# Performance work log

Measured on AMD Instinct MI355X. Metric: run time of the kernel, lower is better.

The kernel has to match this reference:

```python
import jax, jax.numpy as jnp
import numpy as np

DIM = 128
HIDDEN = 512
T_END = 1.0
N_STEPS = 32  # fixed-step RK4 in place of adaptive dopri5


def setup_inputs() -> dict:
    key = jax.random.key(0)
    ks = jax.random.split(key, 8)
    d, h = DIM, HIDDEN
    x = jax.random.normal(ks[0], (65536, d), dtype=jnp.float32)
    # Rademacher probe vector for the Hutchinson trace estimator (fixed per forward pass)
    v = jnp.sign(jax.random.normal(ks[1], (65536, d), dtype=jnp.float32))
    v = jnp.where(v == 0, 1.0, v)
    # ODEF: MLP on concat([z, t]) -> hidden -> hidden -> dim, tanh activations
    s1 = 1.0 / np.sqrt(d + 1)
    s2 = 1.0 / np.sqrt(h)
    W1 = jax.random.uniform(ks[2], (d + 1, h), jnp.float32, -s1, s1)
    b1 = jnp.zeros((h,), jnp.float32)
    W2 = jax.random.uniform(ks[3], (h, h), jnp.float32, -s2, s2)
    b2 = jnp.zeros((h,), jnp.float32)
    W3 = jax.random.uniform(ks[4], (h, d), jnp.float32, -s2, s2)
    b3 = jnp.zeros((d,), jnp.float32)
    return {"x": x, "v": v, "W1": W1, "b1": b1, "W2": W2, "b2": b2, "W3": W3, "b3": b3}


def _mlp(t, z, W1, b1, W2, b2, W3, b3):
    # z: [B, D], t: scalar -> f(z, t): [B, D]
    tt = jnp.full((z.shape[0], 1), t, dtype=z.dtype)
    h = jnp.tanh(jnp.concatenate([z, tt], axis=1) @ W1 + b1)
    h = jnp.tanh(h @ W2 + b2)
    return h @ W3 + b3


def _dynamics(t, z, v, params):
    # returns dz/dt = f and dlogp/dt = -Tr(df/dz) ~= -(v^T J) . v
    f, vjp_fn = jax.vjp(lambda zz: _mlp(t, zz, *params), z)
    (vJ,) = vjp_fn(v)
    div = jnp.sum(vJ * v, axis=1)  # [B]
    return f, -div


def _integrate(x, v, params):
    dt = T_END / N_STEPS
    logp0 = jnp.zeros((x.shape[0],), x.dtype)

    def rk4_step(carry, i):
        z, lp = carry
        t = i.astype(x.dtype) * dt
        k1f, k1d = _dynamics(t, z, v, params)
        k2f, k2d = _dynamics(t + 0.5 * dt, z + 0.5 * dt * k1f, v, params)
        k3f, k3d = _dynamics(t + 0.5 * dt, z + 0.5 * dt * k2f, v, params)
        k4f, k4d = _dynamics(t + dt, z + dt * k3f, v, params)
        z_new = z + (dt / 6.0) * (k1f + 2.0 * k2f + 2.0 * k3f + k4f)
        lp_new = lp + (dt / 6.0) * (k1d + 2.0 * k2d + 2.0 * k3d + k4d)
        return (z_new, lp_new), None

    (zT, logpT), _ = jax.lax.scan(rk4_step, (x, logp0), jnp.arange(N_STEPS))
    return zT, logpT


def reference(x, v, W1, b1, W2, b2, W3, b3):
    params = (W1, b1, W2, b2, W3, b3)
    zT, logpT = _integrate(x, v, params)
    d = x.shape[1]
    log2pi = jnp.asarray(np.log(2.0 * np.pi), x.dtype)
    prior_lp = -0.5 * jnp.sum(zT * zT, axis=1) - 0.5 * d * log2pi  # N(0, I) log-density
    return prior_lp + logpT  # [B] log p(x)
```

## Files before the change

kernel.cpp:

```cpp
#include <hip/hip_runtime.h>


#define DIMV 128
#define HIDV 512
#define HS_STRIDE 520

typedef float  floatx4 __attribute__((ext_vector_type(4)));
typedef short  short8  __attribute__((ext_vector_type(8)));

static __device__ __forceinline__ unsigned short f2bf(float x) {
    union { float f; unsigned int u; } c; c.f = x;
    unsigned int u = c.u;
    u += 0x7FFFu + ((u >> 16) & 1u);
    return (unsigned short)(u >> 16);
}
static __device__ __forceinline__ float bf2f(unsigned short h) {
    union { unsigned int u; float f; } c; c.u = ((unsigned int)h) << 16;
    return c.f;
}
static __device__ __forceinline__ float fast_tanh(float x) {
    x = fminf(8.0f, fmaxf(-8.0f, x));
    float e = exp2f(x * 2.8853900817779268f);
    return (e - 1.0f) * __builtin_amdgcn_rcpf(e + 1.0f);
}

__global__ void pack_kernel(const float* __restrict__ src, unsigned short* __restrict__ dst,
                            int K, int N, int ld, int transpose) {
    int i = blockIdx.x * 256 + threadIdx.x;
    if (i >= K * N) return;
    int j  = i & 7;
    int n  = (i >> 3) % N;
    int k8 = (i >> 3) / N;
    int k  = k8 * 8 + j;
    float v = transpose ? src[n * ld + k] : src[k * ld + n];
    dst[i] = f2bf(v);
}

__global__ void init_k(const float* __restrict__ x, float* __restrict__ z,
                       unsigned short* __restrict__ zs, float* __restrict__ lp,
                       int n, int nrows) {
    int i = blockIdx.x * 256 + threadIdx.x;
    if (i < n) { float val = x[i]; z[i] = val; zs[i] = f2bf(val); }
    if (i < nrows) lp[i] = 0.0f;
}

#define PROD_BF16 0
#define PROD_V    1
#define EPI_H1   0
#define EPI_G3   1

struct GArgs {
    const float* v;
    const unsigned short* A;
    const unsigned short* Wp;
    const float* bias;
    const float* w1t;
    unsigned short* out0;
    float t;
};

template<int KDIM, int NDIM, int NFRAG, int PROD, int EPI>
__global__ __launch_bounds__(256, 2) void gemm_k(GArgs p) {
    __shared__ __align__(16) unsigned short As[128 * 72];
    const int tid  = threadIdx.x;
    const int wave = tid >> 6, lane = tid & 63;
    const int quad = lane >> 4, l16 = lane & 15;
    const int row0 = blockIdx.x * 128;
    const int colw = blockIdx.y * (NFRAG * 64) + wave * (NFRAG * 16);

    floatx4 acc[8][NFRAG];
    #pragma unroll
    for (int m = 0; m < 8; ++m)
        #pragma unroll
        for (int f = 0; f < NFRAG; ++f) {
            floatx4 zz = {0.f, 0.f, 0.f, 0.f};
            acc[m][f] = zz;
        }

    for (int k0 = 0; k0 < KDIM; k0 += 64) {
        __syncthreads();
        {
            const int r  = tid >> 3;
            const int cc = (tid & 7) << 3;
            #pragma unroll
            for (int i = 0; i < 4; ++i) {
                const int rr = r + (i << 5);
                const size_t base = (size_t)(row0 + rr) * KDIM + k0 + cc;
                if constexpr (PROD == PROD_BF16) {
                    const short8 val = *reinterpret_cast<const short8*>(&p.A[base]);
                    *reinterpret_cast<short8*>(&As[rr * 72 + cc]) = val;
                } else {
                    float vals[8];
                    *(float4*)&vals[0] = *(const float4*)&p.v[base];
                    *(float4*)&vals[4] = *(const float4*)&p.v[base + 4];
                    short8 sv;
                    #pragma unroll
                    for (int j = 0; j < 8; ++j) sv[j] = (short)f2bf(vals[j]);
                    *reinterpret_cast<short8*>(&As[rr * 72 + cc]) = sv;
                }
            }
        }
        __syncthreads();
        #pragma unroll
        for (int kt = 0; kt < 2; ++kt) {
            const int k8 = (k0 >> 3) + (kt << 2) + quad;
            short8 b[NFRAG];
            #pragma unroll
            for (int f = 0; f < NFRAG; ++f)
                b[f] = *reinterpret_cast<const short8*>(
                    &p.Wp[((size_t)k8 * NDIM + colw + (f << 4) + l16) << 3]);
            #pragma unroll
            for (int m = 0; m < 8; ++m) {
                const short8 a = *reinterpret_cast<const short8*>(
                    &As[(m * 16 + l16) * 72 + (kt << 5) + (quad << 3)]);
                #pragma unroll
                for (int f = 0; f < NFRAG; ++f)
                    acc[m][f] = __builtin_amdgcn_mfma_f32_16x16x32_bf16(a, b[f], acc[m][f], 0, 0, 0);
            }
        }
    }

    #pragma unroll
    for (int m = 0; m < 8; ++m)
        #pragma unroll
        for (int f = 0; f < NFRAG; ++f) {
            const int col = colw + (f << 4) + l16;
            float bias = 0.0f;
            if constexpr (EPI == EPI_H1) bias = p.bias[col] + p.t * p.w1t[col];
            #pragma unroll
            for (int r = 0; r < 4; ++r) {
                const int row = row0 + m * 16 + quad * 4 + r;
                const size_t idxN = (size_t)row * NDIM + col;
                float x = acc[m][f][r] + bias;
                if constexpr (EPI == EPI_H1) p.out0[idxN] = f2bf(fast_tanh(x));
                else                         p.out0[idxN] = f2bf(x);
            }
        }
}

struct FArgs {
    const unsigned short* A;
    const unsigned short* W2p;
    const unsigned short* W3p;
    const unsigned short* W2Tp;
    const unsigned short* g3;
    const unsigned short* u;
    const float* b2;
    const float* b3;
    float* z;
    float* accf;
    unsigned short* zs;
    float* accd;
    float* lp;
    float cnext, wrk;
    int s0, s3;
};

__global__ __launch_bounds__(512, 4) void kbc_k(FArgs p) {
    __shared__ __align__(16) unsigned short As[64 * 72];
    __shared__ __align__(16) unsigned short Hs[64 * HS_STRIDE];
    const int tid  = threadIdx.x;
    const int wave = tid >> 6, lane = tid & 63;
    const int quad = lane >> 4, l16 = lane & 15;
    const int row0 = blockIdx.x * 64;
    const int colw = wave << 6;

    floatx4 acc[4][4];
    #pragma unroll
    for (int m = 0; m < 4; ++m)
        #pragma unroll
        for (int f = 0; f < 4; ++f) { floatx4 zz = {0.f,0.f,0.f,0.f}; acc[m][f] = zz; }

    const int sr = tid >> 3;
    const int sc = (tid & 7) << 3;
    const unsigned short* Abase = p.A + (size_t)(row0 + sr) * 512 + sc;
    short8 st = *reinterpret_cast<const short8*>(Abase);

    for (int k0 = 0; k0 < 512; k0 += 64) {
        __syncthreads();
        *reinterpret_cast<short8*>(&As[sr * 72 + sc]) = st;
        if (k0 + 64 < 512)
            st = *reinterpret_cast<const short8*>(Abase + k0 + 64);
        __syncthreads();
        #pragma unroll
        for (int kt = 0; kt < 2; ++kt) {
            const int k8 = (k0 >> 3) + (kt << 2) + quad;
            short8 b[4];
            #pragma unroll
            for (int f = 0; f < 4; ++f)
                b[f] = *reinterpret_cast<const short8*>(
                    &p.W2p[((size_t)k8 * 512 + colw + (f << 4) + l16) << 3]);
            #pragma unroll
            for (int m = 0; m < 4; ++m) {
                const short8 a = *reinterpret_cast<const short8*>(
                    &As[(m * 16 + l16) * 72 + (kt << 5) + (quad << 3)]);
                #pragma unroll
                for (int f = 0; f < 4; ++f)
                    acc[m][f] = __builtin_amdgcn_mfma_f32_16x16x32_bf16(a, b[f], acc[m][f], 0, 0, 0);
            }
        }
    }
    #pragma unroll
    for (int m = 0; m < 4; ++m)
        #pragma unroll
        for (int f = 0; f < 4; ++f) {
            const int col = colw + (f << 4) + l16;
            const float bias = p.b2[col];
            #pragma unroll
            for (int r = 0; r < 4; ++r) {
                const int row = m * 16 + quad * 4 + r;
                Hs[row * HS_STRIDE + col] = f2bf(fast_tanh(acc[m][f][r] + bias));
            }
        }
    __syncthreads();

    {
        const int mB   = (wave & 3) << 4;
        const int half = (wave >> 2) << 6;
        floatx4 a3[4];
        #pragma unroll
        for (int f = 0; f < 4; ++f) { floatx4 zz = {0.f,0.f,0.f,0.f}; a3[f] = zz; }
        #pragma unroll 4
        for (int kt = 0; kt < 16; ++kt) {
            const int k8 = (kt << 2) + quad;
            short8 b[4];
            #pragma unroll
            for (int f = 0; f < 4; ++f)
                b[f] = *reinterpret_cast<const short8*>(
                    &p.W3p[((size_t)k8 * 128 + half + (f << 4) + l16) << 3]);
            const short8 a = *reinterpret_cast<const short8*>(
                &Hs[(mB + l16) * HS_STRIDE + (kt << 5) + (quad << 3)]);
            #pragma unroll
            for (int f = 0; f < 4; ++f)
                a3[f] = __builtin_amdgcn_mfma_f32_16x16x32_bf16(a, b[f], a3[f], 0, 0, 0);
        }
        #pragma unroll
        for (int f = 0; f < 4; ++f) {
            const int col = half + (f << 4) + l16;
            const float bias = p.b3[col];
            #pragma unroll
            for (int r = 0; r < 4; ++r) {
                const int row = row0 + mB + quad * 4 + r;
                const size_t idxN = (size_t)row * 128 + col;
                const float x = a3[f][r] + bias;
                const float a = p.wrk * x + (p.s0 ? 0.0f : p.accf[idxN]);
                if (p.s3) {
                    const float zn = p.z[idxN] + a;
                    p.z[idxN]  = zn;
                    p.zs[idxN] = f2bf(zn);
                } else {
                    p.accf[idxN] = a;
                    p.zs[idxN]   = f2bf(p.z[idxN] + p.cnext * x);
                }
            }
        }
    }
    __syncthreads();

    {
        const size_t gbase = (size_t)(row0 + sr) * 512;
        #pragma unroll
        for (int j = 0; j < 8; ++j) {
            const int cc = sc + (j << 6);
            short8 hv = *reinterpret_cast<const short8*>(&Hs[sr * HS_STRIDE + cc]);
            const short8 gv = *reinterpret_cast<const short8*>(&p.g3[gbase + cc]);
            short8 ov;
            #pragma unroll
            for (int e = 0; e < 8; ++e) {
                const float h = bf2f((unsigned short)hv[e]);
                const float g = bf2f((unsigned short)gv[e]);
                ov[e] = (short)f2bf(g * (1.0f - h * h));
            }
            *reinterpret_cast<short8*>(&Hs[sr * HS_STRIDE + cc]) = ov;
        }
    }
    __syncthreads();

    #pragma unroll
    for (int m = 0; m < 4; ++m)
        #pragma unroll
        for (int f = 0; f < 4; ++f) { floatx4 zz = {0.f,0.f,0.f,0.f}; acc[m][f] = zz; }
    #pragma unroll 2
    for (int kt = 0; kt < 16; ++kt) {
        const int k8 = (kt << 2) + quad;
        short8 b[4];
        #pragma unroll
        for (int f = 0; f < 4; ++f)
            b[f] = *reinterpret_cast<const short8*>(
                &p.W2Tp[((size_t)k8 * 512 + colw + (f << 4) + l16) << 3]);
        #pragma unroll
        for (int m = 0; m < 4; ++m) {
            const short8 a = *reinterpret_cast<const short8*>(
                &Hs[(m * 16 + l16) * HS_STRIDE + (kt << 5) + (quad << 3)]);
            #pragma unroll
            for (int f = 0; f < 4; ++f)
                acc[m][f] = __builtin_amdgcn_mfma_f32_16x16x32_bf16(a, b[f], acc[m][f], 0, 0, 0);
        }
    }
    __syncthreads();
    #pragma unroll
    for (int m = 0; m < 4; ++m)
        #pragma unroll
        for (int f = 0; f < 4; ++f) {
            const int col = colw + (f << 4) + l16;
            #pragma unroll
            for (int r = 0; r < 4; ++r) {
                const int row = m * 16 + quad * 4 + r;
                Hs[row * HS_STRIDE + col] = f2bf(acc[m][f][r]);
            }
        }
    __syncthreads();

    {
        const size_t gbase = (size_t)(row0 + sr) * 512;
        float s = 0.0f;
        #pragma unroll
        for (int j = 0; j < 8; ++j) {
            const int cc = sc + (j << 6);
            const short8 xv = *reinterpret_cast<const short8*>(&Hs[sr * HS_STRIDE + cc]);
            const short8 hv = *reinterpret_cast<const short8*>(&p.A[gbase + cc]);
            const short8 uv = *reinterpret_cast<const short8*>(&p.u[gbase + cc]);
            #pragma unroll
            for (int e = 0; e < 8; ++e) {
                const float x = bf2f((unsigned short)xv[e]);
                const float h = bf2f((unsigned short)hv[e]);
                const float uu = bf2f((unsigned short)uv[e]);
                s += x * (1.0f - h * h) * uu;
            }
        }
        s += __shfl_xor(s, 1);
        s += __shfl_xor(s, 2);
        s += __shfl_xor(s, 4);
        if ((tid & 7) == 0) {
            const int row = row0 + sr;
            const float a = p.wrk * (-s) + (p.s0 ? 0.0f : p.accd[row]);
            if (p.s3) p.lp[row] += a;
            else      p.accd[row] = a;
        }
    }
}

__global__ void final_k(const float* __restrict__ z, const float* __restrict__ lp,
                        float* __restrict__ out) {
    const int tid = threadIdx.x;
    const int row = blockIdx.x * 16 + (tid >> 4);
    const int l16 = tid & 15;
    const float4* zr = (const float4*)&z[(size_t)row * 128 + (l16 << 3)];
    float4 a = zr[0], b = zr[1];
    float s = a.x*a.x + a.y*a.y + a.z*a.z + a.w*a.w
            + b.x*b.x + b.y*b.y + b.z*b.z + b.w*b.w;
    s += __shfl_xor(s, 1);
    s += __shfl_xor(s, 2);
    s += __shfl_xor(s, 4);
    s += __shfl_xor(s, 8);
    if (l16 == 0) out[row] = lp[row] - 0.5f * s - 117.6241322501981f;
}

extern "C" void kernel_launch(void* const* d_in, const int* in_sizes, int n_in,
                              void* d_out, int out_size, void* d_ws, size_t ws_size,
                              hipStream_t stream) {
    (void)n_in; (void)out_size;
    const float* x  = (const float*)d_in[0];
    const float* v  = (const float*)d_in[1];
    const float* W1 = (const float*)d_in[2];
    const float* b1 = (const float*)d_in[3];
    const float* W2 = (const float*)d_in[4];
    const float* b2 = (const float*)d_in[5];
    const float* W3 = (const float*)d_in[6];
    const float* b3 = (const float*)d_in[7];
    float* out = (float*)d_out;
    const int B = in_sizes[0] / DIMV;

    auto al = [](size_t s) { return (s + 255) & ~(size_t)255; };
    auto need_for = [&](size_t C) {
        size_t s = 0;
        s += al(C * DIMV * 4);
        s += al(C * DIMV * 4);
        s += al(C * DIMV * 2);
        s += al(C * 4);
        s += al(C * 4);
        s += al(C * HIDV * 2) * 3;
        s += al(128 * 512 * 2) * 3 + al(512 * 512 * 2) * 2;
        return s;
    };
    size_t C = 32768;
    while (C > 1024 && need_for(C) > ws_size) C >>= 1;
    if (need_for(C) > ws_size) return;

    char* w = (char*)d_ws;
    auto alloc = [&](size_t bytes) { char* p = w; w += al(bytes); return p; };
    float* z    = (float*)alloc(C * DIMV * 4);
    float* accf = (float*)alloc(C * DIMV * 4);
    unsigned short* zs = (unsigned short*)alloc(C * DIMV * 2);
    float* lp   = (float*)alloc(C * 4);
    float* accd = (float*)alloc(C * 4);
    unsigned short* h1 = (unsigned short*)alloc(C * HIDV * 2);
    unsigned short* g3 = (unsigned short*)alloc(C * HIDV * 2);
    unsigned short* u  = (unsigned short*)alloc(C * HIDV * 2);
    unsigned short* W1zp  = (unsigned short*)alloc(128 * 512 * 2);
    unsigned short* W3p   = (unsigned short*)alloc(512 * 128 * 2);
    unsigned short* W3Tp  = (unsigned short*)alloc(128 * 512 * 2);
    unsigned short* W2p   = (unsigned short*)alloc(512 * 512 * 2);
    unsigned short* W2Tp  = (unsigned short*)alloc(512 * 512 * 2);

    auto pack = [&](const float* src, unsigned short* dst, int K, int N, int ld, int tr) {
        pack_kernel<<<dim3((K * N + 255) / 256), dim3(256), 0, stream>>>(src, dst, K, N, ld, tr);
    };
    pack(W1, W1zp,  128, 512, 512, 0);
    pack(W2, W2p,   512, 512, 512, 0);
    pack(W3, W3p,   512, 128, 128, 0);
    pack(W2, W2Tp,  512, 512, 512, 1);
    pack(W3, W3Tp,  128, 512, 128, 1);

    const float dt = 1.0f / 32.0f;
    const float cs[4]  = {0.0f, 0.5f * dt, 0.5f * dt, dt};
    const float wr4[4] = {dt / 6.0f, dt / 3.0f, dt / 3.0f, dt / 6.0f};
    const int GM128 = (int)C / 128;
    const int GMF   = (int)C / 64;

    for (int c0 = 0; c0 < B; c0 += (int)C) {
        const float* xc = x + (size_t)c0 * DIMV;
        const float* vc = v + (size_t)c0 * DIMV;

        init_k<<<dim3(((int)C * DIMV + 255) / 256), 256, 0, stream>>>(
            xc, z, zs, lp, (int)C * DIMV, (int)C);

        {
            GArgs p{};
            p.v = vc; p.Wp = W3Tp; p.out0 = g3;
            gemm_k<128, 512, 4, PROD_V, EPI_G3><<<dim3(GM128, 2), 256, 0, stream>>>(p);
            p.Wp = W1zp; p.out0 = u;
            gemm_k<128, 512, 4, PROD_V, EPI_G3><<<dim3(GM128, 2), 256, 0, stream>>>(p);
        }

        for (int step = 0; step < 32; ++step) {
            const float t0 = (float)step * dt;
            for (int s = 0; s < 4; ++s) {
                GArgs p{};
                p.t = t0 + cs[s];
                p.A = zs; p.Wp = W1zp; p.bias = b1; p.w1t = W1 + 128 * 512; p.out0 = h1;
                gemm_k<128, 512, 4, PROD_BF16, EPI_H1><<<dim3(GM128, 2), 256, 0, stream>>>(p);

                FArgs q{};
                q.A = h1; q.W2p = W2p; q.W3p = W3p; q.W2Tp = W2Tp;
                q.g3 = g3; q.u = u; q.b2 = b2; q.b3 = b3;
                q.z = z; q.accf = accf; q.zs = zs; q.accd = accd; q.lp = lp;
                q.cnext = (s < 3) ? cs[s + 1] : 0.0f;
                q.wrk = wr4[s];
                q.s0 = (s == 0); q.s3 = (s == 3);
                kbc_k<<<dim3(GMF), 512, 0, stream>>>(q);
            }
        }

        final_k<<<dim3((int)C / 16), 256, 0, stream>>>(z, lp, out + c0);
    }
}
```

Before: 22.03 ms.

## Fuse all RK4 stages into one persistent ODE kernel per row block

Replaces the 256 per-stage launches (a first-layer GEMM plus a fused backward kernel per RK4 stage) with a single kernel. Each 64-row block runs all 128 stages itself, since rows are independent. The first-layer GEMM now runs inside the block, and the RK accumulators for z and the divergence are held in registers instead of global buffers. This removes launch overhead and the global round-trips for accf/accd. In exchange the grid is fixed at C/64 blocks for the whole integration, W3 is now split per wave by column rather than by row, and h1 is still written to and reread from global memory within the block.

```diff
diff --git a/kernel.cpp b/kernel.cpp
--- a/kernel.cpp
+++ b/kernel.cpp
@@ -37,47 +37,28 @@
 }
 
 __global__ void init_k(const float* __restrict__ x, float* __restrict__ z,
-                       unsigned short* __restrict__ zs, float* __restrict__ lp,
-                       int n, int nrows) {
+                       unsigned short* __restrict__ zs, int n) {
     int i = blockIdx.x * 256 + threadIdx.x;
     if (i < n) { float val = x[i]; z[i] = val; zs[i] = f2bf(val); }
-    if (i < nrows) lp[i] = 0.0f;
-}
-
-#define PROD_BF16 0
-#define PROD_V    1
-#define EPI_H1   0
-#define EPI_G3   1
-
-struct GArgs {
-    const float* v;
-    const unsigned short* A;
-    const unsigned short* Wp;
-    const float* bias;
-    const float* w1t;
-    unsigned short* out0;
-    float t;
-};
-
-template<int KDIM, int NDIM, int NFRAG, int PROD, int EPI>
-__global__ __launch_bounds__(256, 2) void gemm_k(GArgs p) {
+}
+
+__global__ __launch_bounds__(256, 2) void vg_k(const float* __restrict__ v,
+                                               const unsigned short* __restrict__ Wp,
+                                               unsigned short* __restrict__ out0) {
     __shared__ __align__(16) unsigned short As[128 * 72];
     const int tid  = threadIdx.x;
     const int wave = tid >> 6, lane = tid & 63;
     const int quad = lane >> 4, l16 = lane & 15;
     const int row0 = blockIdx.x * 128;
-    const int colw = blockIdx.y * (NFRAG * 64) + wave * (NFRAG * 16);
-
-    floatx4 acc[8][NFRAG];
+    const int colw = blockIdx.y * 256 + wave * 64;
+
+    floatx4 acc[8][4];
     #pragma unroll
     for (int m = 0; m < 8; ++m)
         #pragma unroll
-        for (int f = 0; f < NFRAG; ++f) {
-            floatx4 zz = {0.f, 0.f, 0.f, 0.f};
-            acc[m][f] = zz;
-        }
-
-    for (int k0 = 0; k0 < KDIM; k0 += 64) {
+        for (int f = 0; f < 4; ++f) { floatx4 zz = {0.f,0.f,0.f,0.f}; acc[m][f] = zz; }
+
+    for (int k0 = 0; k0 < 128; k0 += 64) {
         __syncthreads();
         {
             const int r  = tid >> 3;
@@ -85,78 +66,66 @@
             #pragma unroll
             for (int i = 0; i < 4; ++i) {
                 const int rr = r + (i << 5);
-                const size_t base = (size_t)(row0 + rr) * KDIM + k0 + cc;
-                if constexpr (PROD == PROD_BF16) {
-                    const short8 val = *reinterpret_cast<const short8*>(&p.A[base]);
-                    *reinterpret_cast<short8*>(&As[rr * 72 + cc]) = val;
-                } else {
-                    float vals[8];
-                    *(float4*)&vals[0] = *(const float4*)&p.v[base];
-                    *(float4*)&vals[4] = *(const float4*)&p.v[base + 4];
-                    short8 sv;
-                    #pragma unroll
-                    for (int j = 0; j < 8; ++j) sv[j] = (short)f2bf(vals[j]);
-                    *reinterpret_cast<short8*>(&As[rr * 72 + cc]) = sv;
-                }
+                const size_t base = (size_t)(row0 + rr) * 128 + k0 + cc;
+                float vals[8];
+                *(float4*)&vals[0] = *(const float4*)&v[base];
+                *(float4*)&vals[4] = *(const float4*)&v[base + 4];
+                short8 sv;
+                #pragma unroll
+                for (int j = 0; j < 8; ++j) sv[j] = (short)f2bf(vals[j]);
+                *reinterpret_cast<short8*>(&As[rr * 72 + cc]) = sv;
             }
         }
         __syncthreads();
         #pragma unroll
         for (int kt = 0; kt < 2; ++kt) {
             const int k8 = (k0 >> 3) + (kt << 2) + quad;
-            short8 b[NFRAG];
-            #pragma unroll
-            for (int f = 0; f < NFRAG; ++f)
+            short8 b[4];
+            #pragma unroll
+            for (int f = 0; f < 4; ++f)
                 b[f] = *reinterpret_cast<const short8*>(
-                    &p.Wp[((size_t)k8 * NDIM + colw + (f << 4) + l16) << 3]);
+                    &Wp[((size_t)k8 * 512 + colw + (f << 4) + l16) << 3]);
             #pragma unroll
             for (int m = 0; m < 8; ++m) {
                 const short8 a = *reinterpret_cast<const short8*>(
                     &As[(m * 16 + l16) * 72 + (kt << 5) + (quad << 3)]);
                 #pragma unroll
-                for (int f = 0; f < NFRAG; ++f)
+                for (int f = 0; f < 4; ++f)
                     acc[m][f] = __builtin_amdgcn_mfma_f32_16x16x32_bf16(a, b[f], acc[m][f], 0, 0, 0);
             }
         }
     }
-
     #pragma unroll
     for (int m = 0; m < 8; ++m)
         #pragma unroll
-        for (int f = 0; f < NFRAG; ++f) {
+        for (int f = 0; f < 4; ++f) {
             const int col = colw + (f << 4) + l16;
-            float bias = 0.0f;
-            if constexpr (EPI == EPI_H1) bias = p.bias[col] + p.t * p.w1t[col];
             #pragma unroll
             for (int r = 0; r < 4; ++r) {
                 const int row = row0 + m * 16 + quad * 4 + r;
-                const size_t idxN = (size_t)row * NDIM + col;
-                float x = acc[m][f][r] + bias;
-                if constexpr (EPI == EPI_H1) p.out0[idxN] = f2bf(fast_tanh(x));
-                else                         p.out0[idxN] = f2bf(x);
-            }
-        }
-}
-
-struct FArgs {
-    const unsigned short* A;
+                out0[(size_t)row * 512 + col] = f2bf(acc[m][f][r]);
+            }
+        }
+}
+
+struct OArgs {
+    const unsigned short* W1zp;
     const unsigned short* W2p;
     const unsigned short* W3p;
     const unsigned short* W2Tp;
     const unsigned short* g3;
     const unsigned short* u;
+    const float* b1;
+    const float* w1t;
     const float* b2;
     const float* b3;
+    unsigned short* h1;
+    unsigned short* zs;
     float* z;
-    float* accf;
-    unsigned short* zs;
-    float* accd;
     float* lp;
-    float cnext, wrk;
-    int s0, s3;
 };
 
-__global__ __launch_bounds__(512, 4) void kbc_k(FArgs p) {
+__global__ __launch_bounds__(512, 4) void ode_k(OArgs p) {
     __shared__ __align__(16) unsigned short As[64 * 72];
     __shared__ __align__(16) unsigned short Hs[64 * HS_STRIDE];
     const int tid  = threadIdx.x;
@@ -164,180 +133,246 @@
     const int quad = lane >> 4, l16 = lane & 15;
     const int row0 = blockIdx.x * 64;
     const int colw = wave << 6;
-
-    floatx4 acc[4][4];
-    #pragma unroll
-    for (int m = 0; m < 4; ++m)
-        #pragma unroll
-        for (int f = 0; f < 4; ++f) { floatx4 zz = {0.f,0.f,0.f,0.f}; acc[m][f] = zz; }
-
     const int sr = tid >> 3;
     const int sc = (tid & 7) << 3;
-    const unsigned short* Abase = p.A + (size_t)(row0 + sr) * 512 + sc;
-    short8 st = *reinterpret_cast<const short8*>(Abase);
-
-    for (int k0 = 0; k0 < 512; k0 += 64) {
-        __syncthreads();
-        *reinterpret_cast<short8*>(&As[sr * 72 + sc]) = st;
-        if (k0 + 64 < 512)
-            st = *reinterpret_cast<const short8*>(Abase + k0 + 64);
-        __syncthreads();
+    const size_t gbase = (size_t)(row0 + sr) * 512;
+
+    const float dt = 1.0f / 32.0f;
+    float accf_r[4][4];
+    float accd_r = 0.0f, lp_r = 0.0f;
+
+    for (int e = 0; e < 128; ++e) {
+        const int s = e & 3;
+        const int step = e >> 2;
+        const bool s0 = (s == 0), s3 = (s == 3);
+        const float tph  = (s == 0) ? 0.0f : (s == 3 ? dt : 0.5f * dt);
+        const float t    = (float)step * dt + tph;
+        const float wrk  = (s == 1 || s == 2) ? (dt / 3.0f) : (dt / 6.0f);
+        const float cnext = (s <= 1) ? 0.5f * dt : (s == 2 ? dt : 0.0f);
+
+        {
+            floatx4 acc[4][4];
+            #pragma unroll
+            for (int m = 0; m < 4; ++m)
+                #pragma unroll
+                for (int f = 0; f < 4; ++f) { floatx4 zz = {0.f,0.f,0.f,0.f}; acc[m][f] = zz; }
+            #pragma unroll
+            for (int k0 = 0; k0 < 128; k0 += 64) {
+                __syncthreads();
+                *reinterpret_cast<short8*>(&As[sr * 72 + sc]) =
+                    *reinterpret_cast<const short8*>(&p.zs[(size_t)(row0 + sr) * 128 + k0 + sc]);
+                __syncthreads();
+                #pragma unroll
+                for (int kt = 0; kt < 2; ++kt) {
+                    const int k8 = (k0 >> 3) + (kt << 2) + quad;
+                    short8 b[4];
+                    #pragma unroll
+                    for (int f = 0; f < 4; ++f)
+                        b[f] = *reinterpret_cast<const short8*>(
+                            &p.W1zp[((size_t)k8 * 512 + colw + (f << 4) + l16) << 3]);
+                    #pragma unroll
+                    for (int m = 0; m < 4; ++m) {
+                        const short8 a = *reinterpret_cast<const short8*>(
+                            &As[(m * 16 + l16) * 72 + (kt << 5) + (quad << 3)]);
+                        #pragma unroll
+                        for (int f = 0; f < 4; ++f)
+                            acc[m][f] = __builtin_amdgcn_mfma_f32_16x16x32_bf16(a, b[f], acc[m][f], 0, 0, 0);
+                    }
+                }
+            }
+            #pragma unroll
+            for (int m = 0; m < 4; ++m)
+                #pragma unroll
+                for (int f = 0; f < 4; ++f) {
+                    const int col = colw + (f << 4) + l16;
+                    const float bias = p.b1[col] + t * p.w1t[col];
+                    #pragma unroll
+                    for (int r = 0; r < 4; ++r) {
+                        const int row = row0 + m * 16 + quad * 4 + r;
+                        p.h1[(size_t)row * 512 + col] = f2bf(fast_tanh(acc[m][f][r] + bias));
+                    }
+                }
+        }
+        __threadfence_block();
+        __syncthreads();
+
+        {
+            floatx4 acc[4][4];
+            #pragma unroll
+            for (int m = 0; m < 4; ++m)
+                #pragma unroll
+                for (int f = 0; f < 4; ++f) { floatx4 zz = {0.f,0.f,0.f,0.f}; acc[m][f] = zz; }
+
+            const unsigned short* Abase = p.h1 + gbase + sc;
+            short8 st = *reinterpret_cast<const short8*>(Abase);
+            for (int k0 = 0; k0 < 512; k0 += 64) {
+                __syncthreads();
+                *reinterpret_cast<short8*>(&As[sr * 72 + sc]) = st;
+                if (k0 + 64 < 512)
+                    st = *reinterpret_cast<const short8*>(Abase + k0 + 64);
+                __syncthreads();
+                #pragma unroll
+                for (int kt = 0; kt < 2; ++kt) {
+                    const int k8 = (k0 >> 3) + (kt << 2) + quad;
+                    short8 b[4];
+                    #pragma unroll
+                    for (int f = 0; f < 4; ++f)
+                        b[f] = *reinterpret_cast<const short8*>(
+                            &p.W2p[((size_t)k8 * 512 + colw + (f << 4) + l16) << 3]);
+                    #pragma unroll
+                    for (int m = 0; m < 4; ++m) {
+                        const short8 a = *reinterpret_cast<const short8*>(
+                            &As[(m * 16 + l16) * 72 + (kt << 5) + (quad << 3)]);
+                        #pragma unroll
+                        for (int f = 0; f < 4; ++f)
+                            acc[m][f] = __builtin_amdgcn_mfma_f32_16x16x32_bf16(a, b[f], acc[m][f], 0, 0, 0);
+                    }
+                }
+            }
+            #pragma unroll
+            for (int m = 0; m < 4; ++m)
+                #pragma unroll
+                for (int f = 0; f < 4; ++f) {
+                    const int col = colw + (f << 4) + l16;
+                    const float bias = p.b2[col];
+                    #pragma unroll
+                    for (int r = 0; r < 4; ++r) {
+                        const int row = m * 16 + quad * 4 + r;
+                        Hs[row * HS_STRIDE + col] = f2bf(fast_tanh(acc[m][f][r] + bias));
+                    }
+                }
+        }
+        __syncthreads();
+
+        short8 g3v[8];
         #pragma unroll
-        for (int kt = 0; kt < 2; ++kt) {
-            const int k8 = (k0 >> 3) + (kt << 2) + quad;
-            short8 b[4];
-            #pragma unroll
-            for (int f = 0; f < 4; ++f)
-                b[f] = *reinterpret_cast<const short8*>(
-                    &p.W2p[((size_t)k8 * 512 + colw + (f << 4) + l16) << 3]);
+        for (int j = 0; j < 8; ++j)
+            g3v[j] = *reinterpret_cast<const short8*>(&p.g3[gbase + sc + (j << 6)]);
+        {
+            floatx4 accb[4];
+            #pragma unroll
+            for (int m = 0; m < 4; ++m) { floatx4 zz = {0.f,0.f,0.f,0.f}; accb[m] = zz; }
+            const int colB = (wave << 4) + l16;
+            #pragma unroll 4
+            for (int kt = 0; kt < 16; ++kt) {
+                const int k8 = (kt << 2) + quad;
+                const short8 b = *reinterpret_cast<const short8*>(
+                    &p.W3p[((size_t)k8 * 128 + colB) << 3]);
+                #pragma unroll
+                for (int m = 0; m < 4; ++m) {
+                    const short8 a = *reinterpret_cast<const short8*>(
+                        &Hs[(m * 16 + l16) * HS_STRIDE + (kt << 5) + (quad << 3)]);
+                    accb[m] = __builtin_amdgcn_mfma_f32_16x16x32_bf16(a, b, accb[m], 0, 0, 0);
+                }
+            }
+            const float bias = p.b3[colB];
             #pragma unroll
             for (int m = 0; m < 4; ++m) {
-                const short8 a = *reinterpret_cast<const short8*>(
-                    &As[(m * 16 + l16) * 72 + (kt << 5) + (quad << 3)]);
-                #pragma unroll
-                for (int f = 0; f < 4; ++f)
-                    acc[m][f] = __builtin_amdgcn_mfma_f32_16x16x32_bf16(a, b[f], acc[m][f], 0, 0, 0);
-            }
-        }
-    }
-    #pragma unroll
-    for (int m = 0; m < 4; ++m)
-        #pragma unroll
-        for (int f = 0; f < 4; ++f) {
-            const int col = colw + (f << 4) + l16;
-            const float bias = p.b2[col];
-            #pragma unroll
-            for (int r = 0; r < 4; ++r) {
-                const int row = m * 16 + quad * 4 + r;
-                Hs[row * HS_STRIDE + col] = f2bf(fast_tanh(acc[m][f][r] + bias));
-            }
-        }
-    __syncthreads();
-
-    {
-        const int mB   = (wave & 3) << 4;
-        const int half = (wave >> 2) << 6;
-        floatx4 a3[4];
-        #pragma unroll
-        for (int f = 0; f < 4; ++f) { floatx4 zz = {0.f,0.f,0.f,0.f}; a3[f] = zz; }
-        #pragma unroll 4
-        for (int kt = 0; kt < 16; ++kt) {
-            const int k8 = (kt << 2) + quad;
-            short8 b[4];
-            #pragma unroll
-            for (int f = 0; f < 4; ++f)
-                b[f] = *reinterpret_cast<const short8*>(
-                    &p.W3p[((size_t)k8 * 128 + half + (f << 4) + l16) << 3]);
-            const short8 a = *reinterpret_cast<const short8*>(
-                &Hs[(mB + l16) * HS_STRIDE + (kt << 5) + (quad << 3)]);
-            #pragma unroll
-            for (int f = 0; f < 4; ++f)
-                a3[f] = __builtin_amdgcn_mfma_f32_16x16x32_bf16(a, b[f], a3[f], 0, 0, 0);
-        }
-        #pragma unroll
-        for (int f = 0; f < 4; ++f) {
-            const int col = half + (f << 4) + l16;
-            const float bias = p.b3[col];
-            #pragma unroll
-            for (int r = 0; r < 4; ++r) {
-                const int row = row0 + mB + quad * 4 + r;
-                const size_t idxN = (size_t)row * 128 + col;
-                const float x = a3[f][r] + bias;
-                const float a = p.wrk * x + (p.s0 ? 0.0f : p.accf[idxN]);
-                if (p.s3) {
-                    const float zn = p.z[idxN] + a;
-                    p.z[idxN]  = zn;
-                    p.zs[idxN] = f2bf(zn);
-                } else {
-                    p.accf[idxN] = a;
-                    p.zs[idxN]   = f2bf(p.z[idxN] + p.cnext * x);
-                }
-            }
-        }
-    }
-    __syncthreads();
-
-    {
-        const size_t gbase = (size_t)(row0 + sr) * 512;
+                #pragma unroll
+                for (int r = 0; r < 4; ++r) {
+                    const int row = row0 + m * 16 + quad * 4 + r;
+                    const size_t idxN = (size_t)row * 128 + colB;
+                    const float x = accb[m][r] + bias;
+                    const float a = wrk * x + (s0 ? 0.0f : accf_r[m][r]);
+                    if (s3) {
+                        const float zn = p.z[idxN] + a;
+                        p.z[idxN]  = zn;
+                        p.zs[idxN] = f2bf(zn);
+                    } else {
+                        accf_r[m][r] = a;
+                        p.zs[idxN]   = f2bf(p.z[idxN] + cnext * x);
+                    }
+                }
+            }
+        }
+        __threadfence_block();
+        __syncthreads();
+
         #pragma unroll
         for (int j = 0; j < 8; ++j) {
             const int cc = sc + (j << 6);
-            short8 hv = *reinterpret_cast<const short8*>(&Hs[sr * HS_STRIDE + cc]);
-            const short8 gv = *reinterpret_cast<const short8*>(&p.g3[gbase + cc]);
+            const short8 hv = *reinterpret_cast<const short8*>(&Hs[sr * HS_STRIDE + cc]);
             short8 ov;
             #pragma unroll
-            for (int e = 0; e < 8; ++e) {
-                const float h = bf2f((unsigned short)hv[e]);
-                const float g = bf2f((unsigned short)gv[e]);
-                ov[e] = (short)f2bf(g * (1.0f - h * h));
+            for (int el = 0; el < 8; ++el) {
+                const float h = bf2f((unsigned short)hv[el]);
+                const float g = bf2f((unsigned short)g3v[j][el]);
+                ov[el] = (short)f2bf(g * (1.0f - h * h));
             }
             *reinterpret_cast<short8*>(&Hs[sr * HS_STRIDE + cc]) = ov;
         }
+        __syncthreads();
+
+        {
+            floatx4 acc[4][4];
+            #pragma unroll
+            for (int m = 0; m < 4; ++m)
+                #pragma unroll
+                for (int f = 0; f < 4; ++f) { floatx4 zz = {0.f,0.f,0.f,0.f}; acc[m][f] = zz; }
+            #pragma unroll 2
+            for (int kt = 0; kt < 16; ++kt) {
+                const int k8 = (kt << 2) + quad;
+                short8 b[4];
+                #pragma unroll
+                for (int f = 0; f < 4; ++f)
+                    b[f] = *reinterpret_cast<const short8*>(
+                        &p.W2Tp[((size_t)k8 * 512 + colw + (f << 4) + l16) << 3]);
+                #pragma unroll
+                for (int m = 0; m < 4; ++m) {
+                    const short8 a = *reinterpret_cast<const short8*>(
+                        &Hs[(m * 16 + l16) * HS_STRIDE + (kt << 5) + (quad << 3)]);
+                    #pragma unroll
+                    for (int f = 0; f < 4; ++f)
+                        acc[m][f] = __builtin_amdgcn_mfma_f32_16x16x32_bf16(a, b[f], acc[m][f], 0, 0, 0);
+                }
+            }
+            __syncthreads();
+            #pragma unroll
+            for (int m = 0; m < 4; ++m)
+                #pragma unroll
+                for (int f = 0; f < 4; ++f) {
+                    const int col = colw + (f << 4) + l16;
+                    #pragma unroll
+                    for (int r = 0; r < 4; ++r) {
+                        const int row = m * 16 + quad * 4 + r;
+                        Hs[row * HS_STRIDE + col] = f2bf(acc[m][f][r]);
+                    }
+                }
+        }
+        __syncthreads();
+
+        {
+            float sum = 0.0f;
+            short8 hv = *reinterpret_cast<const short8*>(&p.h1[gbase + sc]);
+            short8 uv = *reinterpret_cast<const short8*>(&p.u[gbase + sc]);
+            #pragma unroll
+            for (int j = 0; j < 8; ++j) {
+                short8 hvn = hv, uvn = uv;
+                if (j < 7) {
+                    hvn = *reinterpret_cast<const short8*>(&p.h1[gbase + sc + ((j + 1) << 6)]);
+                    uvn = *reinterpret_cast<const short8*>(&p.u[gbase + sc + ((j + 1) << 6)]);
+                }
+                const int cc = sc + (j << 6);
+                const short8 xv = *reinterpret_cast<const short8*>(&Hs[sr * HS_STRIDE + cc]);
+                #pragma unroll
+                for (int el = 0; el < 8; ++el) {
+                    const float x = bf2f((unsigned short)xv[el]);
+                    const float h = bf2f((unsigned short)hv[el]);
+                    const float uu = bf2f((unsigned short)uv[el]);
+                    sum += x * (1.0f - h * h) * uu;
+                }
+                hv = hvn; uv = uvn;
+            }
+            sum += __shfl_xor(sum, 1);
+            sum += __shfl_xor(sum, 2);
+            sum += __shfl_xor(sum, 4);
+            const float a = wrk * (-sum) + (s0 ? 0.0f : accd_r);
+            if (s3) lp_r += a;
+            else    accd_r = a;
+        }
     }
-    __syncthreads();
-
-    #pragma unroll
-    for (int m = 0; m < 4; ++m)
-        #pragma unroll
-        for (int f = 0; f < 4; ++f) { floatx4 zz = {0.f,0.f,0.f,0.f}; acc[m][f] = zz; }
-    #pragma unroll 2
-    for (int kt = 0; kt < 16; ++kt) {
-        const int k8 = (kt << 2) + quad;
-        short8 b[4];
-        #pragma unroll
-        for (int f = 0; f < 4; ++f)
-            b[f] = *reinterpret_cast<const short8*>(
-                &p.W2Tp[((size_t)k8 * 512 + colw + (f << 4) + l16) << 3]);
-        #pragma unroll
-        for (int m = 0; m < 4; ++m) {
-            const short8 a = *reinterpret_cast<const short8*>(
-                &Hs[(m * 16 + l16) * HS_STRIDE + (kt << 5) + (quad << 3)]);
-            #pragma unroll
-            for (int f = 0; f < 4; ++f)
-                acc[m][f] = __builtin_amdgcn_mfma_f32_16x16x32_bf16(a, b[f], acc[m][f], 0, 0, 0);
-        }
-    }
-    __syncthreads();
-    #pragma unroll
-    for (int m = 0; m < 4; ++m)
-        #pragma unroll
-        for (int f = 0; f < 4; ++f) {
-            const int col = colw + (f << 4) + l16;
-            #pragma unroll
-            for (int r = 0; r < 4; ++r) {
-                const int row = m * 16 + quad * 4 + r;
-                Hs[row * HS_STRIDE + col] = f2bf(acc[m][f][r]);
-            }
-        }
-    __syncthreads();
-
-    {
-        const size_t gbase = (size_t)(row0 + sr) * 512;
-        float s = 0.0f;
-        #pragma unroll
-        for (int j = 0; j < 8; ++j) {
-            const int cc = sc + (j << 6);
-            const short8 xv = *reinterpret_cast<const short8*>(&Hs[sr * HS_STRIDE + cc]);
-            const short8 hv = *reinterpret_cast<const short8*>(&p.A[gbase + cc]);
-            const short8 uv = *reinterpret_cast<const short8*>(&p.u[gbase + cc]);
-            #pragma unroll
-            for (int e = 0; e < 8; ++e) {
-                const float x = bf2f((unsigned short)xv[e]);
-                const float h = bf2f((unsigned short)hv[e]);
-                const float uu = bf2f((unsigned short)uv[e]);
-                s += x * (1.0f - h * h) * uu;
-            }
-        }
-        s += __shfl_xor(s, 1);
-        s += __shfl_xor(s, 2);
-        s += __shfl_xor(s, 4);
-        if ((tid & 7) == 0) {
-            const int row = row0 + sr;
-            const float a = p.wrk * (-s) + (p.s0 ? 0.0f : p.accd[row]);
-            if (p.s3) p.lp[row] += a;
-            else      p.accd[row] = a;
-        }
-    }
+
+    if ((tid & 7) == 0) p.lp[row0 + sr] = lp_r;
 }
 
 __global__ void final_k(const float* __restrict__ z, const float* __restrict__ lp,
@@ -375,9 +410,7 @@
     auto need_for = [&](size_t C) {
         size_t s = 0;
         s += al(C * DIMV * 4);
-        s += al(C * DIMV * 4);
         s += al(C * DIMV * 2);
-        s += al(C * 4);
         s += al(C * 4);
         s += al(C * HIDV * 2) * 3;
         s += al(128 * 512 * 2) * 3 + al(512 * 512 * 2) * 2;
@@ -390,10 +423,8 @@
     char* w = (char*)d_ws;
     auto alloc = [&](size_t bytes) { char* p = w; w += al(bytes); return p; };
     float* z    = (float*)alloc(C * DIMV * 4);
-    float* accf = (float*)alloc(C * DIMV * 4);
     unsigned short* zs = (unsigned short*)alloc(C * DIMV * 2);
     float* lp   = (float*)alloc(C * 4);
-    float* accd = (float*)alloc(C * 4);
     unsigned short* h1 = (unsigned short*)alloc(C * HIDV * 2);
     unsigned short* g3 = (unsigned short*)alloc(C * HIDV * 2);
     unsigned short* u  = (unsigned short*)alloc(C * HIDV * 2);
@@ -412,9 +443,6 @@
     pack(W2, W2Tp,  512, 512, 512, 1);
     pack(W3, W3Tp,  128, 512, 128, 1);
 
-    const float dt = 1.0f / 32.0f;
-    const float cs[4]  = {0.0f, 0.5f * dt, 0.5f * dt, dt};
-    const float wr4[4] = {dt / 6.0f, dt / 3.0f, dt / 3.0f, dt / 6.0f};
     const int GM128 = (int)C / 128;
     const int GMF   = (int)C / 64;
 
@@ -423,34 +451,17 @@
         const float* vc = v + (size_t)c0 * DIMV;
 
         init_k<<<dim3(((int)C * DIMV + 255) / 256), 256, 0, stream>>>(
-            xc, z, zs, lp, (int)C * DIMV, (int)C);
-
-        {
-            GArgs p{};
-            p.v = vc; p.Wp = W3Tp; p.out0 = g3;
-            gemm_k<128, 512, 4, PROD_V, EPI_G3><<<dim3(GM128, 2), 256, 0, stream>>>(p);
-            p.Wp = W1zp; p.out0 = u;
-            gemm_k<128, 512, 4, PROD_V, EPI_G3><<<dim3(GM128, 2), 256, 0, stream>>>(p);
-        }
-
-        for (int step = 0; step < 32; ++step) {
-            const float t0 = (float)step * dt;
-            for (int s = 0; s < 4; ++s) {
-                GArgs p{};
-                p.t = t0 + cs[s];
-                p.A = zs; p.Wp = W1zp; p.bias = b1; p.w1t = W1 + 128 * 512; p.out0 = h1;
-                gemm_k<128, 512, 4, PROD_BF16, EPI_H1><<<dim3(GM128, 2), 256, 0, stream>>>(p);
-
-                FArgs q{};
-                q.A = h1; q.W2p = W2p; q.W3p = W3p; q.W2Tp = W2Tp;
-                q.g3 = g3; q.u = u; q.b2 = b2; q.b3 = b3;
-                q.z = z; q.accf = accf; q.zs = zs; q.accd = accd; q.lp = lp;
-                q.cnext = (s < 3) ? cs[s + 1] : 0.0f;
-                q.wrk = wr4[s];
-                q.s0 = (s == 0); q.s3 = (s == 3);
-                kbc_k<<<dim3(GMF), 512, 0, stream>>>(q);
-            }
-        }
+            xc, z, zs, (int)C * DIMV);
+
+        vg_k<<<dim3(GM128, 2), 256, 0, stream>>>(vc, W3Tp, g3);
+        vg_k<<<dim3(GM128, 2), 256, 0, stream>>>(vc, W1zp, u);
+
+        OArgs q{};
+        q.W1zp = W1zp; q.W2p = W2p; q.W3p = W3p; q.W2Tp = W2Tp;
+        q.g3 = g3; q.u = u;
+        q.b1 = b1; q.w1t = W1 + 128 * 512; q.b2 = b2; q.b3 = b3;
+        q.h1 = h1; q.zs = zs; q.z = z; q.lp = lp;
+        ode_k<<<dim3(GMF), 512, 0, stream>>>(q);
 
         final_k<<<dim3((int)C / 16), 256, 0, stream>>>(z, lp, out + c0);
     }
```

New measurement: 34.54 ms. 1.57x slower.
